# Kernel optimization log

Measured on AMD Instinct MI355X. Metric: run time of the kernel, lower is better.

Reference implementation:

```python
import jax, jax.numpy as jnp
import numpy as np
from itertools import permutations

T, N, C = 8192, 4, 2048
NC = N * C
N_FACT = 24  # 4!


def _build_perm_mat(n):
    perms = list(permutations(range(n)))
    mats = np.zeros((len(perms), n * n), dtype=np.float32)
    for i, perm in enumerate(perms):
        for row, col in enumerate(perm):
            mats[i, row * n + col] = 1.0
    return jnp.asarray(mats)


def setup_inputs() -> dict:
    key = jax.random.key(0)
    k1, k2, k3 = jax.random.split(key, 3)
    x_streams = jax.random.normal(k1, (T, N, C), dtype=jnp.float32)
    W_all = jax.random.normal(k2, (2 * N + N_FACT, NC), dtype=jnp.float32) / np.sqrt(NC)
    b_all = jnp.zeros((2 * N + N_FACT,), dtype=jnp.float32)
    alpha = jnp.full((1,), 0.01, dtype=jnp.float32)
    W_layer = jax.random.normal(k3, (C, C), dtype=jnp.float32) / np.sqrt(C)
    b_layer = jnp.zeros((C,), dtype=jnp.float32)
    return {
        "x_streams": x_streams,
        "W_all": W_all,
        "b_all": b_all,
        "alpha_pre": alpha,
        "alpha_post": alpha,
        "alpha_res": alpha,
        "perm_mat": _build_perm_mat(N),
        "W_layer": W_layer,
        "b_layer": b_layer,
    }


def _mhc_block(x_streams, W_all, b_all, alpha_pre, alpha_post, alpha_res, perm_mat, W_layer, b_layer):
    n = N
    eps = jnp.finfo(x_streams.dtype).eps  # F.rms_norm default eps
    # --- coefficient computation ---
    x_flat = x_streams.reshape(T, NC)                       # (T, n*C)
    inv_rms = jax.lax.rsqrt(jnp.mean(x_flat * x_flat, axis=-1, keepdims=True) + eps)
    x_norm = x_flat * inv_rms
    all_proj = x_norm @ W_all.T                             # (T, 2n + n!)
    pre_proj = all_proj[:, :n]
    post_proj = all_proj[:, n:2 * n]
    res_proj = all_proj[:, 2 * n:]
    h_pre = jax.nn.sigmoid(alpha_pre * pre_proj + b_all[:n])            # (T, n)
    h_post = 2.0 * jax.nn.sigmoid(alpha_post * post_proj + b_all[n:2 * n])  # (T, n)
    a_res = jax.nn.softmax(alpha_res * res_proj + b_all[2 * n:], axis=-1)   # (T, n!)
    H_res = (a_res @ perm_mat).reshape(T, n, n)             # soft permutation
    H_merged = H_res - h_post[:, :, None] * h_pre[:, None, :]  # (T, n, n)
    # --- pre map: mix streams into a single (T, C) layer input ---
    layer_input = jnp.einsum("tn,tnc->tc", h_pre, x_streams)
    # --- wrapped layer: Linear(C, C) ---
    layer_output = layer_input @ W_layer.T + b_layer        # (T, C)
    # --- post + residual ---
    out = jnp.einsum("tnm,tmc->tnc", H_merged, x_streams) + h_post[:, :, None] * layer_output[:, None, :]
    return out


def reference(x_streams, W_all, b_all, alpha_pre, alpha_post, alpha_res, perm_mat, W_layer, b_layer):
    return _mhc_block(x_streams, W_all, b_all, alpha_pre, alpha_post, alpha_res, perm_mat, W_layer, b_layer)
```

## Files before the change

### kernel.cpp

```cpp
#include <hip/hip_runtime.h>

typedef __attribute__((ext_vector_type(8))) short bf16x8;
typedef __attribute__((ext_vector_type(4))) float f32x4;

#if defined(__has_builtin)
#if __has_builtin(__builtin_amdgcn_global_load_lds)
#define HAVE_GLL 1
#endif
#endif

__device__ __forceinline__ ushort f2bf(float f) {
    unsigned u = __float_as_uint(f);
    u += 0x7fffu + ((u >> 16) & 1u);
    return (ushort)(u >> 16);
}

__device__ __forceinline__ void stage16(const ushort* __restrict__ g, ushort* lbase, int lane) {
#ifdef HAVE_GLL
    __builtin_amdgcn_global_load_lds((const __attribute__((address_space(1))) void*)g,
                                     (__attribute__((address_space(3))) void*)lbase,
                                     16, 0, 0);
#else
    *(float4*)(lbase + lane * 8) = *(const float4*)g;
#endif
}

__global__ void k_cvt(const float* __restrict__ src, ushort* __restrict__ dst, int n4) {
    int i = blockIdx.x * blockDim.x + threadIdx.x;
    if (i >= n4) return;
    float4 v = ((const float4*)src)[i];
    ushort4 o;
    o.x = f2bf(v.x); o.y = f2bf(v.y); o.z = f2bf(v.z); o.w = f2bf(v.w);
    ((ushort4*)dst)[i] = o;
}

__global__ __launch_bounds__(512) void k_stats(
    const float* __restrict__ x,
    const ushort* __restrict__ wallb,
    const float* __restrict__ b_all,
    const float* __restrict__ a_pre, const float* __restrict__ a_post,
    const float* __restrict__ a_res,
    const float* __restrict__ perm,
    float* __restrict__ params,
    ushort* __restrict__ li)
{
    __shared__ float dots[8][16][33];
    __shared__ float ssq_s[8][16];
    __shared__ float hpre_l[16][4];

    const int tid = threadIdx.x;
    const int lane = tid & 63;
    const int wq = tid >> 6;
    const int r = lane & 15;
    const int kg = lane >> 4;
    const int brow = blockIdx.x * 16;

    const float* xp = x + (size_t)(brow + r) * 8192 + wq * 1024 + kg * 8;
    const ushort* wp0 = wallb + (size_t)r * 8192 + wq * 1024 + kg * 8;
    const ushort* wp1 = wp0 + 16 * 8192;

    f32x4 acc0 = {}, acc1 = {};
    float ssq = 0.f;

#pragma unroll 4
    for (int s = 0; s < 32; ++s) {
        const int off = s * 32;
        float4 a0 = *(const float4*)(xp + off);
        float4 a1 = *(const float4*)(xp + off + 4);
        float va[8] = {a0.x, a0.y, a0.z, a0.w, a1.x, a1.y, a1.z, a1.w};
        union { ushort u[8]; bf16x8 v; } av;
#pragma unroll
        for (int j = 0; j < 8; ++j) { ssq += va[j] * va[j]; av.u[j] = f2bf(va[j]); }
        bf16x8 b0 = *(const bf16x8*)(wp0 + off);
        bf16x8 b1 = *(const bf16x8*)(wp1 + off);
        acc0 = __builtin_amdgcn_mfma_f32_16x16x32_bf16(av.v, b0, acc0, 0, 0, 0);
        acc1 = __builtin_amdgcn_mfma_f32_16x16x32_bf16(av.v, b1, acc1, 0, 0, 0);
    }

    ssq += __shfl_xor(ssq, 16);
    ssq += __shfl_xor(ssq, 32);
    if (lane < 16) ssq_s[wq][r] = ssq;
#pragma unroll
    for (int i = 0; i < 4; ++i) {
        dots[wq][kg * 4 + i][r] = acc0[i];
        dots[wq][kg * 4 + i][16 + r] = acc1[i];
    }
    __syncthreads();

    if (tid < 16) {
        float s = 0.f;
#pragma unroll
        for (int q = 0; q < 8; ++q) s += ssq_s[q][tid];
        float inv_rms = rsqrtf(s * (1.0f / 8192.0f) + 1.1920929e-7f);
        float pj[32];
#pragma unroll
        for (int j = 0; j < 32; ++j) {
            float d = 0.f;
#pragma unroll
            for (int q = 0; q < 8; ++q) d += dots[q][tid][j];
            pj[j] = d * inv_rms;
        }
        float ap = a_pre[0], apo = a_post[0], ar = a_res[0];
        float hpre[4], hpost[4];
#pragma unroll
        for (int n = 0; n < 4; ++n) {
            hpre[n] = 1.0f / (1.0f + expf(-(ap * pj[n] + b_all[n])));
            hpost[n] = 2.0f / (1.0f + expf(-(apo * pj[4 + n] + b_all[4 + n])));
        }
        float z[24]; float mx = -1e30f;
#pragma unroll
        for (int p = 0; p < 24; ++p) { z[p] = ar * pj[8 + p] + b_all[8 + p]; mx = fmaxf(mx, z[p]); }
        float se = 0.f;
#pragma unroll
        for (int p = 0; p < 24; ++p) { z[p] = expf(z[p] - mx); se += z[p]; }
        float isum = 1.0f / se;
        float Hr[16];
#pragma unroll
        for (int e = 0; e < 16; ++e) Hr[e] = 0.f;
#pragma unroll
        for (int p = 0; p < 24; ++p) {
            float a = z[p] * isum;
#pragma unroll
            for (int e = 0; e < 16; ++e) Hr[e] += a * perm[p * 16 + e];
        }
        float* P = params + (size_t)(brow + tid) * 24;
#pragma unroll
        for (int n = 0; n < 4; ++n) { P[n] = hpre[n]; P[4 + n] = hpost[n]; hpre_l[tid][n] = hpre[n]; }
#pragma unroll
        for (int n = 0; n < 4; ++n)
#pragma unroll
            for (int m = 0; m < 4; ++m)
                P[8 + n * 4 + m] = Hr[n * 4 + m] - hpost[n] * hpre[m];
    }
    __syncthreads();

    const int c = tid * 4;
#pragma unroll 2
    for (int rr = 0; rr < 16; ++rr) {
        float h0 = hpre_l[rr][0], h1 = hpre_l[rr][1], h2 = hpre_l[rr][2], h3 = hpre_l[rr][3];
        const float* xr = x + (size_t)(brow + rr) * 8192 + c;
        float4 a0 = *(const float4*)(xr);
        float4 a1 = *(const float4*)(xr + 2048);
        float4 a2 = *(const float4*)(xr + 4096);
        float4 a3 = *(const float4*)(xr + 6144);
        ushort4 ob;
        ob.x = f2bf(h0 * a0.x + h1 * a1.x + h2 * a2.x + h3 * a3.x);
        ob.y = f2bf(h0 * a0.y + h1 * a1.y + h2 * a2.y + h3 * a3.y);
        ob.z = f2bf(h0 * a0.z + h1 * a1.z + h2 * a2.z + h3 * a3.z);
        ob.w = f2bf(h0 * a0.w + h1 * a1.w + h2 * a2.w + h3 * a3.w);
        *(ushort4*)(li + (size_t)(brow + rr) * 2048 + c) = ob;
    }
}

__global__ __launch_bounds__(256) void k_gemm_out(
    const ushort* __restrict__ liA,
    const ushort* __restrict__ WB,
    const float* __restrict__ b_layer,
    const float* __restrict__ params,
    const float* __restrict__ x,
    float* __restrict__ out)
{
    __shared__ __align__(16) ushort ABlds[4][128 * 64];
    __shared__ float Plds[128 * 25];
    __shared__ float bl_s[128];

    const int tid = threadIdx.x;
    const int ln = tid & 63;
    const int wv = tid >> 6;
    const int brow = blockIdx.x * 128;
    const int bcol = blockIdx.y * 128;

    for (int i = tid; i < 128 * 24; i += 256) {
        int r = i / 24, j = i - r * 24;
        Plds[r * 25 + j] = params[(size_t)(brow + r) * 24 + j];
    }
    if (tid < 128) bl_s[tid] = b_layer[bcol + tid];

    f32x4 acc[4][4] = {};

    const int srow = ln >> 3;
    const int scol = ((ln & 7) ^ srow) * 8;
    const int wm = wv >> 1, wn = wv & 1;
    const int fr = ln & 15, fq = ln >> 4;
    const int swz = (fr & 7) << 3;

    auto do_stage = [&](int buf, int k0) {
#pragma unroll
        for (int q = 0; q < 4; ++q) {
            int row = wv * 32 + q * 8 + srow;
            stage16(liA + (size_t)(brow + row) * 2048 + k0 + scol, &ABlds[buf][wv * 2048 + q * 512], ln);
            stage16(WB + (size_t)(bcol + row) * 2048 + k0 + scol, &ABlds[2 + buf][wv * 2048 + q * 512], ln);
        }
    };

    do_stage(0, 0);
    __syncthreads();

    int cur = 0;
    for (int k0 = 0; k0 < 2048; k0 += 64) {
        if (k0 + 64 < 2048) do_stage(cur ^ 1, k0 + 64);
#pragma unroll
        for (int kk = 0; kk < 64; kk += 32) {
            bf16x8 af[4], bg[4];
#pragma unroll
            for (int mi = 0; mi < 4; ++mi)
                af[mi] = *(const bf16x8*)&ABlds[cur][(wm * 64 + mi * 16 + fr) * 64 + ((kk + fq * 8) ^ swz)];
#pragma unroll
            for (int ni = 0; ni < 4; ++ni)
                bg[ni] = *(const bf16x8*)&ABlds[2 + cur][(wn * 64 + ni * 16 + fr) * 64 + ((kk + fq * 8) ^ swz)];
#pragma unroll
            for (int mi = 0; mi < 4; ++mi)
#pragma unroll
                for (int ni = 0; ni < 4; ++ni)
                    acc[mi][ni] = __builtin_amdgcn_mfma_f32_16x16x32_bf16(bg[ni], af[mi], acc[mi][ni], 0, 0, 0);
        }
        __syncthreads();
        cur ^= 1;
    }

    float* lo_lds = (float*)&ABlds[0][0];
#pragma unroll
    for (int mi = 0; mi < 4; ++mi) {
#pragma unroll
        for (int ni = 0; ni < 4; ++ni) {
            const int t_loc = wm * 64 + mi * 16 + fr;
            const int c_loc = wn * 64 + ni * 16 + fq * 4;
            float4 bl = *(const float4*)&bl_s[c_loc];
            float4 v;
            v.x = acc[mi][ni][0] + bl.x;
            v.y = acc[mi][ni][1] + bl.y;
            v.z = acc[mi][ni][2] + bl.z;
            v.w = acc[mi][ni][3] + bl.w;
            *(float4*)&lo_lds[t_loc * 128 + c_loc] = v;
        }
    }
    __syncthreads();

    const int half = ln >> 5;
    const int cl = (ln & 31) * 4;
    for (int rr = 0; rr < 32; rr += 2) {
        const int t_loc = wv * 32 + rr + half;
        const size_t t = (size_t)(brow + t_loc);
        float4 lo4 = *(const float4*)&lo_lds[t_loc * 128 + cl];
        const float* P = &Plds[t_loc * 25];
        const float* xt = x + t * 8192 + bcol + cl;
        float* ot = out + t * 8192 + bcol + cl;
        float4 x0 = *(const float4*)(xt);
        float4 x1 = *(const float4*)(xt + 2048);
        float4 x2 = *(const float4*)(xt + 4096);
        float4 x3 = *(const float4*)(xt + 6144);
#pragma unroll
        for (int n = 0; n < 4; ++n) {
            float hp = P[4 + n];
            float h0 = P[8 + n * 4 + 0], h1 = P[8 + n * 4 + 1];
            float h2 = P[8 + n * 4 + 2], h3 = P[8 + n * 4 + 3];
            float4 v;
            v.x = hp * lo4.x + h0 * x0.x + h1 * x1.x + h2 * x2.x + h3 * x3.x;
            v.y = hp * lo4.y + h0 * x0.y + h1 * x1.y + h2 * x2.y + h3 * x3.y;
            v.z = hp * lo4.z + h0 * x0.z + h1 * x1.z + h2 * x2.z + h3 * x3.z;
            v.w = hp * lo4.w + h0 * x0.w + h1 * x1.w + h2 * x2.w + h3 * x3.w;
            *(float4*)(ot + (size_t)n * 2048) = v;
        }
    }
}

extern "C" void kernel_launch(void* const* d_in, const int* in_sizes, int n_in,
                              void* d_out, int out_size, void* d_ws, size_t ws_size,
                              hipStream_t stream) {
    const float* x       = (const float*)d_in[0];
    const float* W_all   = (const float*)d_in[1];
    const float* b_all   = (const float*)d_in[2];
    const float* a_pre   = (const float*)d_in[3];
    const float* a_post  = (const float*)d_in[4];
    const float* a_res   = (const float*)d_in[5];
    const float* perm    = (const float*)d_in[6];
    const float* W_layer = (const float*)d_in[7];
    const float* b_layer = (const float*)d_in[8];
    float* out = (float*)d_out;

    char* ws = (char*)d_ws;
    ushort* wall_b   = (ushort*)(ws);
    ushort* wlayer_b = (ushort*)(ws + (512u << 10));
    float*  params   = (float*)(ws + (512u << 10) + (8u << 20));
    ushort* li       = (ushort*)(ws + (512u << 10) + (8u << 20) + (768u << 10));

    k_cvt<<<dim3(256), dim3(256), 0, stream>>>(W_all, wall_b, 65536);
    k_cvt<<<dim3(4096), dim3(256), 0, stream>>>(W_layer, wlayer_b, 1048576);
    k_stats<<<dim3(512), dim3(512), 0, stream>>>(x, wall_b, b_all, a_pre, a_post, a_res,
                                                 perm, params, li);
    k_gemm_out<<<dim3(64, 16), dim3(256), 0, stream>>>(li, wlayer_b, b_layer, params, x, out);
}
```

Baseline: 335.7 us.

## Single-buffer GEMM LDS and split epilogue into halves to raise occupancy

Cuts the GEMM's LDS tiles from double to single buffering. This drops the prefetch overlap and adds a barrier per k-step. The epilogue now stages the output tile through LDS in two 64-row halves with an XOR swizzle, so the smaller buffer suffices and bank conflicts drop. The goal is lower LDS use per block so more blocks fit per CU, at the cost of losing load/compute overlap inside a block.

Result: slower. 401.7 us (+19.7%).

```diff
diff --git a/kernel.cpp b/kernel.cpp
--- a/kernel.cpp
+++ b/kernel.cpp
@@ -160,7 +160,7 @@
     const float* __restrict__ x,
     float* __restrict__ out)
 {
-    __shared__ __align__(16) ushort ABlds[4][128 * 64];
+    __shared__ __align__(16) ushort ABlds[2][128 * 64];
     __shared__ float Plds[128 * 25];
     __shared__ float bl_s[128];
 
@@ -184,83 +184,87 @@
     const int fr = ln & 15, fq = ln >> 4;
     const int swz = (fr & 7) << 3;
 
-    auto do_stage = [&](int buf, int k0) {
+    for (int k0 = 0; k0 < 2048; k0 += 64) {
+        __syncthreads();
 #pragma unroll
         for (int q = 0; q < 4; ++q) {
             int row = wv * 32 + q * 8 + srow;
-            stage16(liA + (size_t)(brow + row) * 2048 + k0 + scol, &ABlds[buf][wv * 2048 + q * 512], ln);
-            stage16(WB + (size_t)(bcol + row) * 2048 + k0 + scol, &ABlds[2 + buf][wv * 2048 + q * 512], ln);
-        }
-    };
-
-    do_stage(0, 0);
-    __syncthreads();
-
-    int cur = 0;
-    for (int k0 = 0; k0 < 2048; k0 += 64) {
-        if (k0 + 64 < 2048) do_stage(cur ^ 1, k0 + 64);
+            stage16(liA + (size_t)(brow + row) * 2048 + k0 + scol, &ABlds[0][wv * 2048 + q * 512], ln);
+            stage16(WB + (size_t)(bcol + row) * 2048 + k0 + scol, &ABlds[1][wv * 2048 + q * 512], ln);
+        }
+        __syncthreads();
 #pragma unroll
         for (int kk = 0; kk < 64; kk += 32) {
             bf16x8 af[4], bg[4];
 #pragma unroll
             for (int mi = 0; mi < 4; ++mi)
-                af[mi] = *(const bf16x8*)&ABlds[cur][(wm * 64 + mi * 16 + fr) * 64 + ((kk + fq * 8) ^ swz)];
+                af[mi] = *(const bf16x8*)&ABlds[0][(wm * 64 + mi * 16 + fr) * 64 + ((kk + fq * 8) ^ swz)];
 #pragma unroll
             for (int ni = 0; ni < 4; ++ni)
-                bg[ni] = *(const bf16x8*)&ABlds[2 + cur][(wn * 64 + ni * 16 + fr) * 64 + ((kk + fq * 8) ^ swz)];
+                bg[ni] = *(const bf16x8*)&ABlds[1][(wn * 64 + ni * 16 + fr) * 64 + ((kk + fq * 8) ^ swz)];
 #pragma unroll
             for (int mi = 0; mi < 4; ++mi)
 #pragma unroll
                 for (int ni = 0; ni < 4; ++ni)
                     acc[mi][ni] = __builtin_amdgcn_mfma_f32_16x16x32_bf16(bg[ni], af[mi], acc[mi][ni], 0, 0, 0);
         }
-        __syncthreads();
-        cur ^= 1;
-    }
+    }
+    __syncthreads();
 
     float* lo_lds = (float*)&ABlds[0][0];
-#pragma unroll
-    for (int mi = 0; mi < 4; ++mi) {
-#pragma unroll
-        for (int ni = 0; ni < 4; ++ni) {
-            const int t_loc = wm * 64 + mi * 16 + fr;
-            const int c_loc = wn * 64 + ni * 16 + fq * 4;
-            float4 bl = *(const float4*)&bl_s[c_loc];
-            float4 v;
-            v.x = acc[mi][ni][0] + bl.x;
-            v.y = acc[mi][ni][1] + bl.y;
-            v.z = acc[mi][ni][2] + bl.z;
-            v.w = acc[mi][ni][3] + bl.w;
-            *(float4*)&lo_lds[t_loc * 128 + c_loc] = v;
-        }
-    }
-    __syncthreads();
-
     const int half = ln >> 5;
-    const int cl = (ln & 31) * 4;
-    for (int rr = 0; rr < 32; rr += 2) {
-        const int t_loc = wv * 32 + rr + half;
-        const size_t t = (size_t)(brow + t_loc);
-        float4 lo4 = *(const float4*)&lo_lds[t_loc * 128 + cl];
-        const float* P = &Plds[t_loc * 25];
-        const float* xt = x + t * 8192 + bcol + cl;
-        float* ot = out + t * 8192 + bcol + cl;
-        float4 x0 = *(const float4*)(xt);
-        float4 x1 = *(const float4*)(xt + 2048);
-        float4 x2 = *(const float4*)(xt + 4096);
-        float4 x3 = *(const float4*)(xt + 6144);
-#pragma unroll
-        for (int n = 0; n < 4; ++n) {
-            float hp = P[4 + n];
-            float h0 = P[8 + n * 4 + 0], h1 = P[8 + n * 4 + 1];
-            float h2 = P[8 + n * 4 + 2], h3 = P[8 + n * 4 + 3];
-            float4 v;
-            v.x = hp * lo4.x + h0 * x0.x + h1 * x1.x + h2 * x2.x + h3 * x3.x;
-            v.y = hp * lo4.y + h0 * x0.y + h1 * x1.y + h2 * x2.y + h3 * x3.y;
-            v.z = hp * lo4.z + h0 * x0.z + h1 * x1.z + h2 * x2.z + h3 * x3.z;
-            v.w = hp * lo4.w + h0 * x0.w + h1 * x1.w + h2 * x2.w + h3 * x3.w;
-            *(float4*)(ot + (size_t)n * 2048) = v;
-        }
+    const int lc32 = ln & 31;
+
+#pragma unroll
+    for (int h = 0; h < 2; ++h) {
+        if (wm == h) {
+#pragma unroll
+            for (int mi = 0; mi < 4; ++mi) {
+#pragma unroll
+                for (int ni = 0; ni < 4; ++ni) {
+                    const int rl = mi * 16 + fr;
+                    const int c_loc = wn * 64 + ni * 16 + fq * 4;
+                    const int slot = (((c_loc >> 2) ^ (rl & 7)) << 2);
+                    float4 bl = *(const float4*)&bl_s[c_loc];
+                    float4 v;
+                    v.x = acc[mi][ni][0] + bl.x;
+                    v.y = acc[mi][ni][1] + bl.y;
+                    v.z = acc[mi][ni][2] + bl.z;
+                    v.w = acc[mi][ni][3] + bl.w;
+                    *(float4*)&lo_lds[rl * 128 + slot] = v;
+                }
+            }
+        }
+        __syncthreads();
+
+#pragma unroll 2
+        for (int rr = 0; rr < 16; rr += 2) {
+            const int rl2 = wv * 16 + rr + half;
+            const int t_loc = h * 64 + rl2;
+            const size_t t = (size_t)(brow + t_loc);
+            const int c_act = ((lc32 ^ (rl2 & 7)) << 2);
+            float4 lo4 = *(const float4*)&lo_lds[rl2 * 128 + (lc32 << 2)];
+            const float* P = &Plds[t_loc * 25];
+            const float* xt = x + t * 8192 + bcol + c_act;
+            float* ot = out + t * 8192 + bcol + c_act;
+            float4 x0 = *(const float4*)(xt);
+            float4 x1 = *(const float4*)(xt + 2048);
+            float4 x2 = *(const float4*)(xt + 4096);
+            float4 x3 = *(const float4*)(xt + 6144);
+#pragma unroll
+            for (int n = 0; n < 4; ++n) {
+                float hp = P[4 + n];
+                float h0 = P[8 + n * 4 + 0], h1 = P[8 + n * 4 + 1];
+                float h2 = P[8 + n * 4 + 2], h3 = P[8 + n * 4 + 3];
+                float4 v;
+                v.x = hp * lo4.x + h0 * x0.x + h1 * x1.x + h2 * x2.x + h3 * x3.x;
+                v.y = hp * lo4.y + h0 * x0.y + h1 * x1.y + h2 * x2.y + h3 * x3.y;
+                v.z = hp * lo4.z + h0 * x0.z + h1 * x1.z + h2 * x2.z + h3 * x3.z;
+                v.w = hp * lo4.w + h0 * x0.w + h1 * x1.w + h2 * x2.w + h3 * x3.w;
+                *(float4*)(ot + (size_t)n * 2048) = v;
+            }
+        }
+        __syncthreads();
     }
 }
 
```
